# Optimization experiments

Measured on AMD Instinct MI355X. Metric: run time of the kernel, lower is better.

Reference implementation:

```python
import jax, jax.numpy as jnp
import numpy as np

B, T, S, D, H, DH = 2, 2048, 2048, 1024, 16, 64
LN_EPS = 1e-5


def setup_inputs() -> dict:
    key = jax.random.key(0)
    ks = jax.random.split(key, 8)
    return {
        "x": jax.random.normal(ks[0], (B, T, D), jnp.float32),
        "context": jax.random.normal(ks[1], (B, S, D), jnp.float32),
        "lookup_table": jax.random.normal(ks[2], (2 * T - 1, DH), jnp.float32),
        "Wq": jax.random.normal(ks[3], (D, H * DH), jnp.float32) * 0.02,
        "Wk": jax.random.normal(ks[4], (D, H * DH), jnp.float32) * 0.02,
        "Wv": jax.random.normal(ks[5], (D, H * DH), jnp.float32) * 0.02,
        "Wo": jax.random.normal(ks[6], (H * DH, D), jnp.float32) * 0.02,
        "bo": jnp.zeros((D,), jnp.float32),
        "gamma": jnp.ones((D,), jnp.float32),
        "beta": jnp.zeros((D,), jnp.float32),
    }


def skew(QE):
    # QE: [B, H, T, 2T-1] -> [B, H, T, T] via pad/reshape relative-position trick
    b, h, t, _ = QE.shape
    QE = jnp.pad(QE, ((0, 0), (0, 0), (0, 0), (0, 1))).reshape(b, h, -1)
    QE = jnp.pad(QE, ((0, 0), (0, 0), (0, t - 1))).reshape(b, h, t + 1, 2 * t - 1)
    return QE[:, :, :t, -t:]


def reference(x, context, lookup_table, Wq, Wk, Wv, Wo, bo, gamma, beta):
    scale = 1.0 / jnp.sqrt(jnp.asarray(DH, x.dtype))
    # pre-layernorm on queries
    mu = jnp.mean(x, axis=-1, keepdims=True)
    var = jnp.var(x, axis=-1, keepdims=True)
    xn = (x - mu) / jnp.sqrt(var + LN_EPS) * gamma + beta
    q = (xn @ Wq).reshape(B, T, H, DH).transpose(0, 2, 1, 3)       # [B,H,T,DH]
    k = (context @ Wk).reshape(B, S, H, DH).transpose(0, 2, 1, 3)  # [B,H,S,DH]
    v = (context @ Wv).reshape(B, S, H, DH).transpose(0, 2, 1, 3)  # [B,H,S,DH]
    score = jnp.einsum("bhtd,bhsd->bhts", q, k) * scale            # [B,H,T,S]
    rel = skew(jnp.einsum("bhtd,ld->bhtl", q, lookup_table))       # [B,H,T,T]
    # NOTE: faithful to original — QK^T gets scaled twice, rel term once
    score = (score + rel) * scale
    attn = jax.nn.softmax(score, axis=-1)
    out = jnp.einsum("bhts,bhsd->bhtd", attn, v)
    out = out.transpose(0, 2, 1, 3).reshape(B, T, H * DH)
    out = out @ Wo + bo
    # dropout=0 (eval); residual uses the layernormed x (as in source)
    return xn + out
```

## Files before the change

kernel.cpp:

```cpp
#include <hip/hip_runtime.h>

#define DEVFN __device__ __forceinline__

typedef __bf16 bf16x8 __attribute__((ext_vector_type(8)));
typedef float f32x4 __attribute__((ext_vector_type(4)));
typedef unsigned short u16;


DEVFN u16 f2bf(float f) {
  unsigned u = __builtin_bit_cast(unsigned, f);
  u += 0x7FFFu + ((u >> 16) & 1u);
  return (u16)(u >> 16);
}

DEVFN f32x4 mfma16(bf16x8 a, bf16x8 b, f32x4 c) {
  return __builtin_amdgcn_mfma_f32_16x16x32_bf16(a, b, c, 0, 0, 0);
}

DEVFN void gl16(const u16* g, u16* l) {
  __builtin_amdgcn_global_load_lds(
      (const __attribute__((address_space(1))) unsigned int*)g,
      (__attribute__((address_space(3))) unsigned int*)l, 16, 0, 0);
}

__global__ __launch_bounds__(256) void ln_kernel(const float* __restrict__ x,
                                                 const float* __restrict__ gamma,
                                                 const float* __restrict__ beta,
                                                 float* __restrict__ xn,
                                                 u16* __restrict__ xnb) {
  int row = blockIdx.x;
  int tid = threadIdx.x;
  const float4* xr = (const float4*)(x + (size_t)row * 1024);
  float4 v = xr[tid];
  float s = v.x + v.y + v.z + v.w;
  float q = v.x * v.x + v.y * v.y + v.z * v.z + v.w * v.w;
#pragma unroll
  for (int m = 1; m < 64; m <<= 1) {
    s += __shfl_xor(s, m);
    q += __shfl_xor(q, m);
  }
  __shared__ float rs[4], rq[4];
  int w = tid >> 6;
  if ((tid & 63) == 0) { rs[w] = s; rq[w] = q; }
  __syncthreads();
  s = rs[0] + rs[1] + rs[2] + rs[3];
  q = rq[0] + rq[1] + rq[2] + rq[3];
  float mean = s * (1.0f / 1024.0f);
  float var = q * (1.0f / 1024.0f) - mean * mean;
  float inv = rsqrtf(var + 1e-5f);
  float4 g = ((const float4*)gamma)[tid];
  float4 bt = ((const float4*)beta)[tid];
  float4 o;
  o.x = (v.x - mean) * inv * g.x + bt.x;
  o.y = (v.y - mean) * inv * g.y + bt.y;
  o.z = (v.z - mean) * inv * g.z + bt.z;
  o.w = (v.w - mean) * inv * g.w + bt.w;
  ((float4*)(xn + (size_t)row * 1024))[tid] = o;
  ushort4 ob;
  ob.x = f2bf(o.x); ob.y = f2bf(o.y); ob.z = f2bf(o.z); ob.w = f2bf(o.w);
  ((ushort4*)(xnb + (size_t)row * 1024))[tid] = ob;
}

__global__ __launch_bounds__(256) void cvt_kernel(const float* __restrict__ in,
                                                  u16* __restrict__ out, int n4) {
  int i = blockIdx.x * 256 + threadIdx.x;
  if (i < n4) {
    float4 v = ((const float4*)in)[i];
    ushort4 o;
    o.x = f2bf(v.x); o.y = f2bf(v.y); o.z = f2bf(v.z); o.w = f2bf(v.w);
    ((ushort4*)out)[i] = o;
  }
}

__global__ __launch_bounds__(256) void transW_kernel(const float* __restrict__ W0,
                                                     const float* __restrict__ W1,
                                                     const float* __restrict__ W2,
                                                     const float* __restrict__ W3,
                                                     u16* __restrict__ Wall) {
  __shared__ float tile[32][33];
  int z = blockIdx.z;
  const float* W = (z == 0) ? W0 : (z == 1) ? W1 : (z == 2) ? W2 : W3;
  float scale = (z == 0) ? 0.18033688011112042f : (z == 1) ? 0.125f : 1.0f;
  u16* Wt = Wall + (size_t)z * 1048576;
  int tx = threadIdx.x, ty = threadIdx.y;
  int x = blockIdx.x * 32 + tx;
  int y0 = blockIdx.y * 32;
#pragma unroll
  for (int j = 0; j < 32; j += 8)
    tile[ty + j][tx] = W[(size_t)(y0 + ty + j) * 1024 + x];
  __syncthreads();
#pragma unroll
  for (int j = 0; j < 32; j += 8)
    Wt[(size_t)(blockIdx.x * 32 + ty + j) * 1024 + y0 + tx] = f2bf(tile[tx][ty + j] * scale);
}

DEVFN void gemm_core(const u16* __restrict__ A, const u16* __restrict__ Bt,
                     u16* Ab, u16* Bb, int row0, int n0, int tid,
                     f32x4 (&acc)[2][4]) {
  int lane = tid & 63, wv = tid >> 6;
  int l16 = lane & 15, lhi = lane >> 4;
  int r8 = lane >> 3, c8 = lane & 7;
  int cx = ((c8 ^ r8) << 3);
  int swz = (l16 & 7) << 3;

  auto stage = [&](int k0) {
#pragma unroll
    for (int i = 0; i < 4; ++i) {
      int rowb = wv * 32 + i * 8;
      gl16(&A[(size_t)(row0 + rowb + r8) * 1024 + k0 + cx], &Ab[rowb * 64]);
    }
#pragma unroll
    for (int i = 0; i < 2; ++i) {
      int rowb = wv * 16 + i * 8;
      gl16(&Bt[(size_t)(n0 + rowb + r8) * 1024 + k0 + cx], &Bb[rowb * 64]);
    }
  };

  stage(0);
  asm volatile("s_waitcnt vmcnt(0)" ::: "memory");
  __syncthreads();
  for (int kk = 0; kk < 16; ++kk) {
    __builtin_amdgcn_s_setprio(1);
#pragma unroll
    for (int ks = 0; ks < 2; ++ks) {
      bf16x8 af[2], bfr[4];
#pragma unroll
      for (int mi = 0; mi < 2; ++mi) {
        int row = wv * 32 + mi * 16 + l16;
        af[mi] = *(const bf16x8*)&Ab[row * 64 + ((ks * 32 + lhi * 8) ^ swz)];
      }
#pragma unroll
      for (int ni = 0; ni < 4; ++ni) {
        int row = ni * 16 + l16;
        bfr[ni] = *(const bf16x8*)&Bb[row * 64 + ((ks * 32 + lhi * 8) ^ swz)];
      }
#pragma unroll
      for (int mi = 0; mi < 2; ++mi)
#pragma unroll
        for (int ni = 0; ni < 4; ++ni)
          acc[mi][ni] = mfma16(af[mi], bfr[ni], acc[mi][ni]);
    }
    __builtin_amdgcn_s_setprio(0);
    if (kk < 15) {
      __syncthreads();
      stage((kk + 1) * 64);
      asm volatile("s_waitcnt vmcnt(0)" ::: "memory");
      __syncthreads();
    }
  }
}

__global__ __launch_bounds__(256, 4) void qkv_kernel(const u16* __restrict__ xnb,
                                                     const u16* __restrict__ ctxb,
                                                     const u16* __restrict__ Wall,
                                                     u16* __restrict__ qb,
                                                     u16* __restrict__ kb,
                                                     u16* __restrict__ vtb) {
  __shared__ __align__(16) u16 Ab[128 * 64];
  __shared__ __align__(16) u16 Bb[64 * 64];
  int z = blockIdx.z;
  const u16* A = (z == 0) ? xnb : ctxb;
  const u16* Bt = Wall + (size_t)z * 1048576;
  int row0 = blockIdx.x * 128, n0 = blockIdx.y * 64;
  f32x4 acc[2][4] = {};
  gemm_core(A, Bt, Ab, Bb, row0, n0, threadIdx.x, acc);
  int tid = threadIdx.x, lane = tid & 63, wv = tid >> 6;
  int l16 = lane & 15, lhi = lane >> 4;
  u16* qk = (z == 0) ? qb : kb;
#pragma unroll
  for (int mi = 0; mi < 2; ++mi)
#pragma unroll
    for (int ni = 0; ni < 4; ++ni)
#pragma unroll
      for (int r = 0; r < 4; ++r) {
        int m = row0 + wv * 32 + mi * 16 + lhi * 4 + r;
        int n = n0 + ni * 16 + l16;
        int b = m >> 11, t = m & 2047, h = n >> 6, dh = n & 63;
        u16 val = f2bf(acc[mi][ni][r]);
        if (z < 2)
          qk[(size_t)((b * 16 + h) * 2048 + t) * 64 + dh] = val;
        else
          vtb[(size_t)((b * 16 + h) * 64 + dh) * 2048 + t] = val;
      }
}

__global__ __launch_bounds__(256, 4) void oproj_kernel(const u16* __restrict__ attnb,
                                                       const u16* __restrict__ Wall,
                                                       const float* __restrict__ bias,
                                                       const float* __restrict__ resid,
                                                       float* __restrict__ outF) {
  __shared__ __align__(16) u16 Ab[128 * 64];
  __shared__ __align__(16) u16 Bb[64 * 64];
  const u16* Bt = Wall + (size_t)3 * 1048576;
  int row0 = blockIdx.x * 128, n0 = blockIdx.y * 64;
  f32x4 acc[2][4] = {};
  gemm_core(attnb, Bt, Ab, Bb, row0, n0, threadIdx.x, acc);
  int tid = threadIdx.x, lane = tid & 63, wv = tid >> 6;
  int l16 = lane & 15, lhi = lane >> 4;
#pragma unroll
  for (int mi = 0; mi < 2; ++mi)
#pragma unroll
    for (int ni = 0; ni < 4; ++ni)
#pragma unroll
      for (int r = 0; r < 4; ++r) {
        int m = row0 + wv * 32 + mi * 16 + lhi * 4 + r;
        int n = n0 + ni * 16 + l16;
        outF[(size_t)m * 1024 + n] = acc[mi][ni][r] + bias[n] + resid[(size_t)m * 1024 + n];
      }
}

__global__ __launch_bounds__(256, 4) void flash_kernel(
    const u16* __restrict__ Qg, const u16* __restrict__ Kg,
    const u16* __restrict__ Vtg, const u16* __restrict__ Lb,
    u16* __restrict__ Og) {
  constexpr int T = 2048, H = 16;
  int p = blockIdx.x;
  int bid = (p & 7) * 128 + (p >> 3);
  int qb = bid & 31, h = (bid >> 5) & 15, b = bid >> 9;
  int tid = threadIdx.x;
  int lane = tid & 63, w = tid >> 6;
  int l16 = lane & 15, lhi = lane >> 4;

  __shared__ __align__(16) u16 Klds[64 * 64];
  __shared__ __align__(16) u16 Vt[64 * 64];
  __shared__ __align__(16) u16 Llds[128 * 64];
  __shared__ __align__(16) u16 Plds[4][16 * 64];

  const u16* qbase = Qg + (size_t)(b * H + h) * T * 64;
  const u16* kbase = Kg + (size_t)(b * H + h) * T * 64;
  const u16* vtbase = Vtg + (size_t)(b * H + h) * 64 * 2048;

  int i0b = qb * 64;
  int i0w = i0b + w * 16;
  bf16x8 aq[2];
  aq[0] = *(const bf16x8*)&qbase[(i0w + l16) * 64 + lhi * 8];
  aq[1] = *(const bf16x8*)&qbase[(i0w + l16) * 64 + 32 + lhi * 8];

  f32x4 accO[4] = {};
  float mrun[4], lsum[4];
#pragma unroll
  for (int r = 0; r < 4; ++r) { mrun[r] = -1e30f; lsum[r] = 0.0f; }

  int bandbase = T - 16 - i0w;
  int ubase0 = T - 64 - i0b;
  int uoff = 48 - 16 * w;

  int r8 = lane >> 3, c8 = lane & 7;
  int cx = ((c8 ^ r8) << 3);
  int swz = (l16 & 7) << 3;

  auto stageKL = [&](int j0) {
#pragma unroll
    for (int i = 0; i < 2; ++i) {
      int rowb = w * 16 + i * 8;
      gl16(&kbase[(size_t)(j0 + rowb + r8) * 64 + cx], &Klds[rowb * 64]);
    }
#pragma unroll
    for (int i = 0; i < 4; ++i) {
      int rowb = w * 32 + i * 8;
      gl16(&Lb[(size_t)(ubase0 + j0 + rowb + r8) * 64 + cx], &Llds[rowb * 64]);
    }
  };
  auto stageV = [&](int j0) {
#pragma unroll
    for (int i = 0; i < 2; ++i) {
      int rowb = w * 16 + i * 8;
      gl16(&vtbase[(size_t)(rowb + r8) * 2048 + j0 + cx], &Vt[rowb * 64]);
    }
  };

  const u16* lp = Lb + (size_t)(bandbase + l16) * 64 + lhi * 8;
  f32x4 eC = {};
#pragma unroll
  for (int ks = 0; ks < 2; ++ks)
    eC = mfma16(aq[ks], *(const bf16x8*)&lp[ks * 32], eC);

  f32x4 accS[4];
  f32x4 accE[5];
  auto computeQKE = [&]() {
#pragma unroll
    for (int kb = 0; kb < 4; ++kb) accS[kb] = f32x4{0.f, 0.f, 0.f, 0.f};
    accE[0] = eC;
#pragma unroll
    for (int c = 1; c < 5; ++c) accE[c] = f32x4{0.f, 0.f, 0.f, 0.f};
    __builtin_amdgcn_s_setprio(1);
#pragma unroll
    for (int ks = 0; ks < 2; ++ks) {
#pragma unroll
      for (int kb = 0; kb < 4; ++kb) {
        int row = kb * 16 + l16;
        bf16x8 bk = *(const bf16x8*)&Klds[row * 64 + ((ks * 32 + lhi * 8) ^ swz)];
        accS[kb] = mfma16(aq[ks], bk, accS[kb]);
      }
#pragma unroll
      for (int c = 1; c < 5; ++c) {
        int urow = uoff + c * 16 + l16;
        bf16x8 bl = *(const bf16x8*)&Llds[urow * 64 + ((ks * 32 + lhi * 8) ^ swz)];
        accE[c] = mfma16(aq[ks], bl, accE[c]);
      }
    }
    __builtin_amdgcn_s_setprio(0);
    eC = accE[4];
  };

  const float THR = 11.541560327111707f;

  stageKL(0);
  asm volatile("s_waitcnt vmcnt(0)" ::: "memory");
  __syncthreads();
  stageV(0);
  computeQKE();

  for (int kt = 0; kt < 32; ++kt) {
    __syncthreads();
    if (kt < 31) stageKL((kt + 1) * 64);
    __builtin_amdgcn_sched_barrier(0);

    float sc[4][4];
    float lm[4];
    bool need = false;
#pragma unroll
    for (int r = 0; r < 4; ++r) {
      int m = lhi * 4 + r;
      int srcl = lhi * 16 + ((l16 - m + 15) & 15);
      bool lo = (l16 <= m);
      float e[5];
#pragma unroll
      for (int c = 0; c < 5; ++c) e[c] = __shfl(accE[c][r], srcl);
#pragma unroll
      for (int kb = 0; kb < 4; ++kb) sc[r][kb] = accS[kb][r] + (lo ? e[kb] : e[kb + 1]);
      lm[r] = fmaxf(fmaxf(sc[r][0], sc[r][1]), fmaxf(sc[r][2], sc[r][3]));
      need |= (lm[r] > mrun[r] + THR);
    }
    if (__ballot(need)) {
#pragma unroll
      for (int r = 0; r < 4; ++r) {
        float tm = lm[r];
        tm = fmaxf(tm, __shfl_xor(tm, 1));
        tm = fmaxf(tm, __shfl_xor(tm, 2));
        tm = fmaxf(tm, __shfl_xor(tm, 4));
        tm = fmaxf(tm, __shfl_xor(tm, 8));
        float mnew = fmaxf(mrun[r], tm);
        float al = exp2f(mrun[r] - mnew);
        mrun[r] = mnew;
        lsum[r] *= al;
#pragma unroll
        for (int dt = 0; dt < 4; ++dt) accO[dt][r] *= al;
      }
    }
#pragma unroll
    for (int r = 0; r < 4; ++r) {
      int m = lhi * 4 + r;
      int swm = (m & 7) << 3;
      float mm = mrun[r];
      float pv0 = exp2f(sc[r][0] - mm);
      float pv1 = exp2f(sc[r][1] - mm);
      float pv2 = exp2f(sc[r][2] - mm);
      float pv3 = exp2f(sc[r][3] - mm);
      lsum[r] += (pv0 + pv1) + (pv2 + pv3);
      unsigned pk01, pk23;
      asm("v_cvt_pk_bf16_f32 %0, %1, %2" : "=v"(pk01) : "v"(pv0), "v"(pv1));
      asm("v_cvt_pk_bf16_f32 %0, %1, %2" : "=v"(pk23) : "v"(pv2), "v"(pv3));
      Plds[w][m * 64 + ((l16) ^ swm)] = (u16)pk01;
      Plds[w][m * 64 + ((16 + l16) ^ swm)] = (u16)(pk01 >> 16);
      Plds[w][m * 64 + ((32 + l16) ^ swm)] = (u16)pk23;
      Plds[w][m * 64 + ((48 + l16) ^ swm)] = (u16)(pk23 >> 16);
    }

    __builtin_amdgcn_s_setprio(1);
#pragma unroll
    for (int ks = 0; ks < 2; ++ks) {
      bf16x8 ap = *(const bf16x8*)&Plds[w][l16 * 64 + ((ks * 32 + lhi * 8) ^ swz)];
#pragma unroll
      for (int dt = 0; dt < 4; ++dt) {
        int row = dt * 16 + l16;
        bf16x8 bv = *(const bf16x8*)&Vt[row * 64 + ((ks * 32 + lhi * 8) ^ swz)];
        accO[dt] = mfma16(ap, bv, accO[dt]);
      }
    }
    __builtin_amdgcn_s_setprio(0);

    __syncthreads();
    if (kt < 31) {
      stageV((kt + 1) * 64);
      __builtin_amdgcn_sched_barrier(0);
      computeQKE();
    }
  }

#pragma unroll
  for (int r = 0; r < 4; ++r) {
    float l = lsum[r];
    l += __shfl_xor(l, 1);
    l += __shfl_xor(l, 2);
    l += __shfl_xor(l, 4);
    l += __shfl_xor(l, 8);
    lsum[r] = 1.0f / l;
  }
#pragma unroll
  for (int dt = 0; dt < 4; ++dt)
#pragma unroll
    for (int r = 0; r < 4; ++r) {
      int i = i0w + lhi * 4 + r;
      int col = h * 64 + dt * 16 + l16;
      Og[(size_t)(b * T + i) * 1024 + col] = f2bf(accO[dt][r] * lsum[r]);
    }
}

extern "C" void kernel_launch(void* const* d_in, const int* in_sizes, int n_in,
                              void* d_out, int out_size, void* d_ws, size_t ws_size,
                              hipStream_t stream) {
  const float* x = (const float*)d_in[0];
  const float* ctx = (const float*)d_in[1];
  const float* Ltab = (const float*)d_in[2];
  const float* Wq = (const float*)d_in[3];
  const float* Wk = (const float*)d_in[4];
  const float* Wv = (const float*)d_in[5];
  const float* Wo = (const float*)d_in[6];
  const float* bo = (const float*)d_in[7];
  const float* gamma = (const float*)d_in[8];
  const float* beta = (const float*)d_in[9];
  float* out = (float*)d_out;

  size_t off = 0;
  auto take = [&](size_t bytes) {
    void* p = (char*)d_ws + off;
    off += (bytes + 255) & ~(size_t)255;
    return p;
  };
  u16* xnb = (u16*)take(8388608);
  u16* ctxb = (u16*)take(8388608);
  u16* Lb = (u16*)take(4095 * 64 * 2);
  u16* Wall = (u16*)take(4 * 2097152);
  u16* qbuf = (u16*)take(8388608);
  u16* kbuf = (u16*)take(8388608);
  u16* vtbuf = (u16*)take(8388608);
  u16* attnb = (u16*)take(8388608);

  ln_kernel<<<dim3(4096), dim3(256), 0, stream>>>(x, gamma, beta, out, xnb);
  cvt_kernel<<<dim3(4096), dim3(256), 0, stream>>>(ctx, ctxb, 1048576);
  cvt_kernel<<<dim3(256), dim3(256), 0, stream>>>(Ltab, Lb, 65520);
  transW_kernel<<<dim3(32, 32, 4), dim3(32, 8), 0, stream>>>(Wq, Wk, Wv, Wo, Wall);
  qkv_kernel<<<dim3(32, 16, 3), dim3(256), 0, stream>>>(xnb, ctxb, Wall, qbuf, kbuf, vtbuf);
  flash_kernel<<<dim3(1024), dim3(256), 0, stream>>>(qbuf, kbuf, vtbuf, Lb, attnb);
  oproj_kernel<<<dim3(32, 16), dim3(256), 0, stream>>>(attnb, Wall, bo, out, out);
}
```

Measured before the change: 202.4 us.

## Permute V key order so P tile stores as one 8-byte write; merge cvt launches

The V projection epilogue now writes V^T with key positions permuted inside each 64-key block. Each lane's four P values become contiguous in LDS, so the flash kernel stores them with a single 8-byte write instead of four scattered 2-byte writes. The P and V^T columns are permuted identically, so the PV product is unchanged. Separately, the two float-to-bf16 conversion launches (context and lookup table) are merged into one kernel to save a launch. The risks are new LDS bank conflicts from the changed swizzle and less coalesced global writes in the qkv epilogue.

```diff
diff --git a/kernel.cpp b/kernel.cpp
--- a/kernel.cpp
+++ b/kernel.cpp
@@ -61,14 +61,25 @@
   ((ushort4*)(xnb + (size_t)row * 1024))[tid] = ob;
 }
 
-__global__ __launch_bounds__(256) void cvt_kernel(const float* __restrict__ in,
-                                                  u16* __restrict__ out, int n4) {
-  int i = blockIdx.x * 256 + threadIdx.x;
-  if (i < n4) {
-    float4 v = ((const float4*)in)[i];
+__global__ __launch_bounds__(256) void cvt2_kernel(const float* __restrict__ a,
+                                                   u16* __restrict__ oa,
+                                                   const float* __restrict__ bsrc,
+                                                   u16* __restrict__ ob) {
+  int blk = blockIdx.x;
+  if (blk < 4096) {
+    int i = blk * 256 + threadIdx.x;
+    float4 v = ((const float4*)a)[i];
     ushort4 o;
     o.x = f2bf(v.x); o.y = f2bf(v.y); o.z = f2bf(v.z); o.w = f2bf(v.w);
-    ((ushort4*)out)[i] = o;
+    ((ushort4*)oa)[i] = o;
+  } else {
+    int i = (blk - 4096) * 256 + threadIdx.x;
+    if (i < 65520) {
+      float4 v = ((const float4*)bsrc)[i];
+      ushort4 o;
+      o.x = f2bf(v.x); o.y = f2bf(v.y); o.z = f2bf(v.z); o.w = f2bf(v.w);
+      ((ushort4*)ob)[i] = o;
+    }
   }
 }
 
@@ -177,10 +188,12 @@
         int n = n0 + ni * 16 + l16;
         int b = m >> 11, t = m & 2047, h = n >> 6, dh = n & 63;
         u16 val = f2bf(acc[mi][ni][r]);
-        if (z < 2)
+        if (z < 2) {
           qk[(size_t)((b * 16 + h) * 2048 + t) * 64 + dh] = val;
-        else
-          vtb[(size_t)((b * 16 + h) * 64 + dh) * 2048 + t] = val;
+        } else {
+          int t2 = (t & ~63) | ((t & 15) << 2) | ((t >> 4) & 3);
+          vtb[(size_t)((b * 16 + h) * 64 + dh) * 2048 + t2] = val;
+        }
       }
 }
 
@@ -351,7 +364,6 @@
 #pragma unroll
     for (int r = 0; r < 4; ++r) {
       int m = lhi * 4 + r;
-      int swm = (m & 7) << 3;
       float mm = mrun[r];
       float pv0 = exp2f(sc[r][0] - mm);
       float pv1 = exp2f(sc[r][1] - mm);
@@ -361,10 +373,10 @@
       unsigned pk01, pk23;
       asm("v_cvt_pk_bf16_f32 %0, %1, %2" : "=v"(pk01) : "v"(pv0), "v"(pv1));
       asm("v_cvt_pk_bf16_f32 %0, %1, %2" : "=v"(pk23) : "v"(pv2), "v"(pv3));
-      Plds[w][m * 64 + ((l16) ^ swm)] = (u16)pk01;
-      Plds[w][m * 64 + ((16 + l16) ^ swm)] = (u16)(pk01 >> 16);
-      Plds[w][m * 64 + ((32 + l16) ^ swm)] = (u16)pk23;
-      Plds[w][m * 64 + ((48 + l16) ^ swm)] = (u16)(pk23 >> 16);
+      uint2 pw;
+      pw.x = pk01;
+      pw.y = pk23;
+      *(uint2*)&Plds[w][m * 64 + ((l16 * 4) ^ ((m & 7) << 3))] = pw;
     }
 
     __builtin_amdgcn_s_setprio(1);
@@ -438,8 +450,7 @@
   u16* attnb = (u16*)take(8388608);
 
   ln_kernel<<<dim3(4096), dim3(256), 0, stream>>>(x, gamma, beta, out, xnb);
-  cvt_kernel<<<dim3(4096), dim3(256), 0, stream>>>(ctx, ctxb, 1048576);
-  cvt_kernel<<<dim3(256), dim3(256), 0, stream>>>(Ltab, Lb, 65520);
+  cvt2_kernel<<<dim3(4096 + 256), dim3(256), 0, stream>>>(ctx, ctxb, Ltab, Lb);
   transW_kernel<<<dim3(32, 32, 4), dim3(32, 8), 0, stream>>>(Wq, Wk, Wv, Wo, Wall);
   qkv_kernel<<<dim3(32, 16, 3), dim3(256), 0, stream>>>(xnb, ctxb, Wall, qbuf, kbuf, vtbuf);
   flash_kernel<<<dim3(1024), dim3(256), 0, stream>>>(qbuf, kbuf, vtbuf, Lb, attnb);
```

Result: faster. 192.9 us (-4.7%).
